# Performance work log

Hardware: AMD Instinct MI355X
Metric: run time of the kernel (lower is better)

Reference implementation:

```python
import jax, jax.numpy as jnp
import numpy as np

N_NODES = 50000
N_EDGES = 800000
IN_DIM, HID, EMB = 128, 256, 128


def _gcn_conv(x, src, dst, W, b, n_nodes):
    # PyG GCNConv: add self-loops, symmetric norm D^-1/2 (A+I) D^-1/2, then linear.
    h = x @ W  # [N, out]
    deg = jnp.zeros((n_nodes,), x.dtype).at[dst].add(1.0) + 1.0  # +1 for self-loop
    dinv = jax.lax.rsqrt(deg)
    norm = dinv[src] * dinv[dst]  # [E]
    agg = jnp.zeros_like(h).at[dst].add(h[src] * norm[:, None])
    agg = agg + h * (dinv * dinv)[:, None]  # self-loop term
    return agg + b


def setup_inputs() -> dict:
    key = jax.random.key(0)
    ks = jax.random.split(key, 16)
    s = lambda *sh: None
    x = jax.random.normal(ks[0], (N_NODES, IN_DIM), jnp.float32)
    edge_index = jax.random.randint(ks[1], (2, N_EDGES), 0, N_NODES, jnp.int32)
    def lin(k, fan_in, fan_out):
        lim = 1.0 / np.sqrt(fan_in)
        kw, kb = jax.random.split(k)
        W = jax.random.uniform(kw, (fan_in, fan_out), jnp.float32, -lim, lim)
        b = jax.random.uniform(kb, (fan_out,), jnp.float32, -lim, lim)
        return W, b
    W1, b1 = lin(ks[2], IN_DIM, HID)
    W2, b2 = lin(ks[3], HID, EMB)
    fc1_W, fc1_b = lin(ks[4], EMB, HID)
    fc2_W, fc2_b = lin(ks[5], HID, 1)
    np_W, np_b = lin(ks[6], EMB, 3)
    ep_W, ep_b = lin(ks[7], 2 * EMB, 2)
    gp_W, gp_b = lin(ks[8], EMB, 1)
    return dict(x=x, edge_index=edge_index, W1=W1, b1=b1, W2=W2, b2=b2,
                fc1_W=fc1_W, fc1_b=fc1_b, fc2_W=fc2_W, fc2_b=fc2_b,
                np_W=np_W, np_b=np_b, ep_W=ep_W, ep_b=ep_b, gp_W=gp_W, gp_b=gp_b)


def reference(x, edge_index, W1, b1, W2, b2, fc1_W, fc1_b, fc2_W, fc2_b,
              np_W, np_b, ep_W, ep_b, gp_W, gp_b):
    src, dst = edge_index[0], edge_index[1]
    n = x.shape[0]
    h = jax.nn.relu(_gcn_conv(x, src, dst, W1, b1, n))
    h = jax.nn.relu(_gcn_conv(h, src, dst, W2, b2, n))  # [N, EMB]
    g = jnp.mean(h, axis=0, keepdims=True)  # [1, EMB]
    v = jax.nn.relu(g @ fc1_W + fc1_b)
    value = v @ fc2_W + fc2_b  # [1,1]
    node_logits = h @ np_W + np_b  # [N,3]
    edge_features = jnp.concatenate([h[src], h[dst]], axis=1)  # [E, 2*EMB]
    edge_logits = edge_features @ ep_W + ep_b  # [E,2]
    global_logits = g @ gp_W + gp_b  # [1,1]
    return (node_logits, edge_logits, global_logits, value)
```

## Files before the change

### kernel.cpp

```cpp
#include <hip/hip_runtime.h>
#include <hip/hip_bf16.h>

typedef __attribute__((ext_vector_type(8))) short bf16x8;
typedef __attribute__((ext_vector_type(4))) float f32x4;

__device__ inline unsigned short f2bf(float f) {
    union { float f; unsigned u; } v; v.f = f;
    unsigned r = v.u + 0x7fff + ((v.u >> 16) & 1);
    return (unsigned short)(r >> 16);
}
__device__ inline float bf2f(unsigned short b) {
    union { unsigned u; float f; } v; v.u = ((unsigned)b) << 16;
    return v.f;
}
__device__ inline float bfu_lo(unsigned r) {
    union { unsigned u; float f; } v; v.u = r << 16;
    return v.f;
}
__device__ inline float bfu_hi(unsigned r) {
    union { unsigned u; float f; } v; v.u = r & 0xffff0000u;
    return v.f;
}

__global__ __launch_bounds__(256) void prep_kernel(
    const float* __restrict__ x, unsigned short* __restrict__ xb,
    const float* __restrict__ W1, unsigned short* __restrict__ W1t_hi, unsigned short* __restrict__ W1t_lo,
    const float* __restrict__ W2, unsigned short* __restrict__ W2t_hi, unsigned short* __restrict__ W2t_lo,
    int* __restrict__ zero_ints, float* __restrict__ gsum, int n) {
    int tid = blockIdx.x * blockDim.x + threadIdx.x;
    int C = n * 32;
    if (tid < C) {
        int base = tid * 4;
        float4 v = *(const float4*)&x[base];
        unsigned lo = (unsigned)f2bf(v.x) | ((unsigned)f2bf(v.y) << 16);
        unsigned hi = (unsigned)f2bf(v.z) | ((unsigned)f2bf(v.w) << 16);
        uint2 p; p.x = lo; p.y = hi;
        *(uint2*)&xb[base] = p;
        return;
    }
    tid -= C;
    if (tid < 65536) {
        if (tid < 32768) {
            int k = tid >> 8, j = tid & 255;
            float v = W1[tid];
            unsigned short h = f2bf(v);
            W1t_hi[(size_t)j * 128 + k] = h;
            W1t_lo[(size_t)j * 128 + k] = f2bf(v - bf2f(h));
        } else {
            int i2 = tid - 32768;
            int k = i2 >> 7, j = i2 & 127;
            float v = W2[i2];
            unsigned short h = f2bf(v);
            W2t_hi[(size_t)j * 256 + k] = h;
            W2t_lo[(size_t)j * 256 + k] = f2bf(v - bf2f(h));
        }
        return;
    }
    tid -= 65536;
    if (tid < 2 * n) { zero_ints[tid] = 0; return; }
    tid -= 2 * n;
    if (tid < 128) gsum[tid] = 0.f;
}

__global__ void hist_kernel(const int* __restrict__ dst, int* __restrict__ deg, int nE) {
    int e = blockIdx.x * blockDim.x + threadIdx.x;
    if (e < nE) atomicAdd(&deg[dst[e]], 1);
}

__global__ __launch_bounds__(1024) void scanA_kernel(const int* __restrict__ deg,
                                                     int* __restrict__ local,
                                                     float* __restrict__ dinv,
                                                     int* __restrict__ bsum, int n) {
    __shared__ int wsum[16];
    __shared__ int woff[16];
    int t = threadIdx.x, lane = t & 63, wid = t >> 6;
    int i = blockIdx.x * 1024 + t;
    int val = (i < n) ? deg[i] : 0;
    if (i < n) dinv[i] = rsqrtf((float)(val + 1));
    int inc = val;
    for (int s = 1; s < 64; s <<= 1) {
        int tmp = __shfl_up(inc, s);
        if (lane >= s) inc += tmp;
    }
    if (lane == 63) wsum[wid] = inc;
    __syncthreads();
    if (wid == 0) {
        int w = (lane < 16) ? wsum[lane] : 0;
        for (int s = 1; s < 16; s <<= 1) {
            int tmp = __shfl_up(w, s);
            if (lane >= s) w += tmp;
        }
        if (lane < 16) woff[lane] = w - wsum[lane];
        if (lane == 15) bsum[blockIdx.x] = w;
    }
    __syncthreads();
    if (i < n) local[i] = woff[wid] + (inc - val);
}

__global__ void scanB_kernel(const int* __restrict__ bsum, int* __restrict__ boff, int nb) {
    int lane = threadIdx.x & 63;
    int v = (lane < nb) ? bsum[lane] : 0;
    int inc = v;
    for (int s = 1; s < 64; s <<= 1) {
        int tmp = __shfl_up(inc, s);
        if (lane >= s) inc += tmp;
    }
    if (lane < nb) boff[lane] = inc - v;
}

__global__ void fill_kernel(const int* __restrict__ src, const int* __restrict__ dst,
                            const int* __restrict__ local, const int* __restrict__ boff,
                            int* __restrict__ cnt, const float* __restrict__ dinv,
                            int2* __restrict__ csr, int nE) {
    int e = blockIdx.x * blockDim.x + threadIdx.x;
    if (e >= nE) return;
    int s = src[e], d = dst[e];
    int pos = local[d] + boff[d >> 10] + atomicAdd(&cnt[d], 1);
    float w = dinv[s] * dinv[d];
    csr[pos] = make_int2(s, __float_as_int(w));
}

__global__ __launch_bounds__(256) void gather1_kernel(const unsigned int* __restrict__ xb,
                                                      const int2* __restrict__ csr,
                                                      const int* __restrict__ local,
                                                      const int* __restrict__ boff,
                                                      const int* __restrict__ deg,
                                                      const float* __restrict__ dinv,
                                                      unsigned int* __restrict__ xin_hi,
                                                      unsigned int* __restrict__ xin_lo, int n) {
    int node = blockIdx.x * 4 + (threadIdx.x >> 6);
    int lane = threadIdx.x & 63;
    if (node >= n) return;
    int p = local[node] + boff[node >> 10];
    int e0 = p + deg[node];
    unsigned rs = xb[(size_t)node * 64 + lane];
    float a0 = 0.f, a1 = 0.f, b0 = 0.f, b1 = 0.f;
    float c0 = 0.f, c1 = 0.f, d0v = 0.f, d1v = 0.f;
    for (; p + 7 < e0; p += 8) {
        int2 q0 = csr[p], q1 = csr[p + 1], q2 = csr[p + 2], q3 = csr[p + 3];
        int2 q4 = csr[p + 4], q5 = csr[p + 5], q6 = csr[p + 6], q7 = csr[p + 7];
        unsigned r0 = xb[(size_t)q0.x * 64 + lane];
        unsigned r1 = xb[(size_t)q1.x * 64 + lane];
        unsigned r2 = xb[(size_t)q2.x * 64 + lane];
        unsigned r3 = xb[(size_t)q3.x * 64 + lane];
        unsigned r4 = xb[(size_t)q4.x * 64 + lane];
        unsigned r5 = xb[(size_t)q5.x * 64 + lane];
        unsigned r6 = xb[(size_t)q6.x * 64 + lane];
        unsigned r7 = xb[(size_t)q7.x * 64 + lane];
        float w0 = __int_as_float(q0.y), w1 = __int_as_float(q1.y);
        float w2 = __int_as_float(q2.y), w3 = __int_as_float(q3.y);
        float w4 = __int_as_float(q4.y), w5 = __int_as_float(q5.y);
        float w6 = __int_as_float(q6.y), w7 = __int_as_float(q7.y);
        a0 += w0 * bfu_lo(r0); a1 += w0 * bfu_hi(r0);
        b0 += w1 * bfu_lo(r1); b1 += w1 * bfu_hi(r1);
        c0 += w2 * bfu_lo(r2); c1 += w2 * bfu_hi(r2);
        d0v += w3 * bfu_lo(r3); d1v += w3 * bfu_hi(r3);
        a0 += w4 * bfu_lo(r4); a1 += w4 * bfu_hi(r4);
        b0 += w5 * bfu_lo(r5); b1 += w5 * bfu_hi(r5);
        c0 += w6 * bfu_lo(r6); c1 += w6 * bfu_hi(r6);
        d0v += w7 * bfu_lo(r7); d1v += w7 * bfu_hi(r7);
    }
    for (; p + 3 < e0; p += 4) {
        int2 q0 = csr[p], q1 = csr[p + 1], q2 = csr[p + 2], q3 = csr[p + 3];
        unsigned r0 = xb[(size_t)q0.x * 64 + lane];
        unsigned r1 = xb[(size_t)q1.x * 64 + lane];
        unsigned r2 = xb[(size_t)q2.x * 64 + lane];
        unsigned r3 = xb[(size_t)q3.x * 64 + lane];
        float w0 = __int_as_float(q0.y), w1 = __int_as_float(q1.y);
        float w2 = __int_as_float(q2.y), w3 = __int_as_float(q3.y);
        a0 += w0 * bfu_lo(r0); a1 += w0 * bfu_hi(r0);
        b0 += w1 * bfu_lo(r1); b1 += w1 * bfu_hi(r1);
        c0 += w2 * bfu_lo(r2); c1 += w2 * bfu_hi(r2);
        d0v += w3 * bfu_lo(r3); d1v += w3 * bfu_hi(r3);
    }
    for (; p < e0; ++p) {
        int2 q = csr[p];
        float w = __int_as_float(q.y);
        unsigned r = xb[(size_t)q.x * 64 + lane];
        a0 += w * bfu_lo(r); a1 += w * bfu_hi(r);
    }
    a0 = (a0 + b0) + (c0 + d0v);
    a1 = (a1 + b1) + (c1 + d1v);
    float di = dinv[node];
    float d2 = di * di;
    a0 += d2 * bfu_lo(rs);
    a1 += d2 * bfu_hi(rs);
    unsigned short h0 = f2bf(a0), h1 = f2bf(a1);
    xin_hi[(size_t)node * 64 + lane] = (unsigned)h0 | ((unsigned)h1 << 16);
    unsigned short l0 = f2bf(a0 - bf2f(h0)), l1 = f2bf(a1 - bf2f(h1));
    xin_lo[(size_t)node * 64 + lane] = (unsigned)l0 | ((unsigned)l1 << 16);
}

template <int K, int NOUT, bool BIAS_RELU, bool A_SPLIT>
__global__ __launch_bounds__(256) void mfma_gemm_kernel(
    const unsigned short* __restrict__ Ahi, const unsigned short* __restrict__ Alo,
    const unsigned short* __restrict__ Wthi, const unsigned short* __restrict__ Wtlo,
    const float* __restrict__ bias,
    unsigned short* __restrict__ O, int n) {
    int w = threadIdx.x >> 6, l = threadIdx.x & 63;
    int m0 = blockIdx.x * 128 + w * 32;
    int j0 = blockIdx.y * 64;
    int col16 = l & 15;
    int koff = (l >> 4) * 8;
    int rowA0 = m0 + col16;       if (rowA0 >= n) rowA0 = n - 1;
    int rowA1 = m0 + 16 + col16;  if (rowA1 >= n) rowA1 = n - 1;
    f32x4 acc[2][4];
#pragma unroll
    for (int g = 0; g < 2; ++g)
#pragma unroll
        for (int c = 0; c < 4; ++c) acc[g][c] = (f32x4){0.f, 0.f, 0.f, 0.f};
    for (int k0 = 0; k0 < K; k0 += 32) {
        bf16x8 ah0 = *(const bf16x8*)&Ahi[(size_t)rowA0 * K + k0 + koff];
        bf16x8 ah1 = *(const bf16x8*)&Ahi[(size_t)rowA1 * K + k0 + koff];
        bf16x8 al0, al1;
        if (A_SPLIT) {
            al0 = *(const bf16x8*)&Alo[(size_t)rowA0 * K + k0 + koff];
            al1 = *(const bf16x8*)&Alo[(size_t)rowA1 * K + k0 + koff];
        }
#pragma unroll
        for (int c = 0; c < 4; ++c) {
            size_t wb = (size_t)(j0 + c * 16 + col16) * K + k0 + koff;
            bf16x8 wh = *(const bf16x8*)&Wthi[wb];
            bf16x8 wl = *(const bf16x8*)&Wtlo[wb];
            acc[0][c] = __builtin_amdgcn_mfma_f32_16x16x32_bf16(ah0, wh, acc[0][c], 0, 0, 0);
            if (A_SPLIT) acc[0][c] = __builtin_amdgcn_mfma_f32_16x16x32_bf16(al0, wh, acc[0][c], 0, 0, 0);
            acc[0][c] = __builtin_amdgcn_mfma_f32_16x16x32_bf16(ah0, wl, acc[0][c], 0, 0, 0);
            acc[1][c] = __builtin_amdgcn_mfma_f32_16x16x32_bf16(ah1, wh, acc[1][c], 0, 0, 0);
            if (A_SPLIT) acc[1][c] = __builtin_amdgcn_mfma_f32_16x16x32_bf16(al1, wh, acc[1][c], 0, 0, 0);
            acc[1][c] = __builtin_amdgcn_mfma_f32_16x16x32_bf16(ah1, wl, acc[1][c], 0, 0, 0);
        }
    }
#pragma unroll
    for (int g = 0; g < 2; ++g) {
#pragma unroll
        for (int c = 0; c < 4; ++c) {
            int col = j0 + c * 16 + col16;
#pragma unroll
            for (int r = 0; r < 4; ++r) {
                int orow = m0 + g * 16 + (l >> 4) * 4 + r;
                if (orow >= n) continue;
                float v = acc[g][c][r];
                if (BIAS_RELU) v = fmaxf(v + bias[col], 0.f);
                O[(size_t)orow * NOUT + col] = f2bf(v);
            }
        }
    }
}

__global__ __launch_bounds__(256) void conv2_fused_kernel(
    const unsigned int* __restrict__ h2b, const int2* __restrict__ csr,
    const int* __restrict__ local, const int* __restrict__ boff,
    const int* __restrict__ deg,
    const float* __restrict__ dinv, const float* __restrict__ b2,
    const float* __restrict__ npW, const float* __restrict__ npb,
    const float* __restrict__ epW, const float* __restrict__ epb,
    float* __restrict__ out_nl, float* __restrict__ uv,
    float* __restrict__ gsum, int n) {
    __shared__ float lgs[4][128];
    int lane = threadIdx.x & 63;
    int wid = threadIdx.x >> 6;
    int d0 = lane * 2, d1 = lane * 2 + 1;
    float wn00 = npW[d0 * 3 + 0], wn10 = npW[d0 * 3 + 1], wn20 = npW[d0 * 3 + 2];
    float wn01 = npW[d1 * 3 + 0], wn11 = npW[d1 * 3 + 1], wn21 = npW[d1 * 3 + 2];
    float wu00 = epW[d0 * 2 + 0], wu10 = epW[d0 * 2 + 1];
    float wu01 = epW[d1 * 2 + 0], wu11 = epW[d1 * 2 + 1];
    float wv00 = epW[(d0 + 128) * 2 + 0], wv10 = epW[(d0 + 128) * 2 + 1];
    float wv01 = epW[(d1 + 128) * 2 + 0], wv11 = epW[(d1 + 128) * 2 + 1];
    float b20 = b2[d0], b21 = b2[d1];
    float npb0 = npb[0], npb1 = npb[1], npb2 = npb[2];
    float epb0 = epb[0], epb1 = epb[1];
    float p0 = 0.f, p1 = 0.f;

    for (int node = blockIdx.x * 4 + wid; node < n; node += gridDim.x * 4) {
        int p = local[node] + boff[node >> 10];
        int e0 = p + deg[node];
        unsigned rs = h2b[(size_t)node * 64 + lane];
        float a0 = 0.f, a1 = 0.f, b0 = 0.f, b1 = 0.f;
        float c0 = 0.f, c1 = 0.f, e0v = 0.f, e1v = 0.f;
        for (; p + 7 < e0; p += 8) {
            int2 q0 = csr[p], q1 = csr[p + 1], q2 = csr[p + 2], q3 = csr[p + 3];
            int2 q4 = csr[p + 4], q5 = csr[p + 5], q6 = csr[p + 6], q7 = csr[p + 7];
            unsigned r0 = h2b[(size_t)q0.x * 64 + lane];
            unsigned r1 = h2b[(size_t)q1.x * 64 + lane];
            unsigned r2 = h2b[(size_t)q2.x * 64 + lane];
            unsigned r3 = h2b[(size_t)q3.x * 64 + lane];
            unsigned r4 = h2b[(size_t)q4.x * 64 + lane];
            unsigned r5 = h2b[(size_t)q5.x * 64 + lane];
            unsigned r6 = h2b[(size_t)q6.x * 64 + lane];
            unsigned r7 = h2b[(size_t)q7.x * 64 + lane];
            float w0 = __int_as_float(q0.y), w1 = __int_as_float(q1.y);
            float w2 = __int_as_float(q2.y), w3 = __int_as_float(q3.y);
            float w4 = __int_as_float(q4.y), w5 = __int_as_float(q5.y);
            float w6 = __int_as_float(q6.y), w7 = __int_as_float(q7.y);
            a0 += w0 * bfu_lo(r0); a1 += w0 * bfu_hi(r0);
            b0 += w1 * bfu_lo(r1); b1 += w1 * bfu_hi(r1);
            c0 += w2 * bfu_lo(r2); c1 += w2 * bfu_hi(r2);
            e0v += w3 * bfu_lo(r3); e1v += w3 * bfu_hi(r3);
            a0 += w4 * bfu_lo(r4); a1 += w4 * bfu_hi(r4);
            b0 += w5 * bfu_lo(r5); b1 += w5 * bfu_hi(r5);
            c0 += w6 * bfu_lo(r6); c1 += w6 * bfu_hi(r6);
            e0v += w7 * bfu_lo(r7); e1v += w7 * bfu_hi(r7);
        }
        for (; p + 3 < e0; p += 4) {
            int2 q0 = csr[p], q1 = csr[p + 1], q2 = csr[p + 2], q3 = csr[p + 3];
            unsigned r0 = h2b[(size_t)q0.x * 64 + lane];
            unsigned r1 = h2b[(size_t)q1.x * 64 + lane];
            unsigned r2 = h2b[(size_t)q2.x * 64 + lane];
            unsigned r3 = h2b[(size_t)q3.x * 64 + lane];
            float w0 = __int_as_float(q0.y), w1 = __int_as_float(q1.y);
            float w2 = __int_as_float(q2.y), w3 = __int_as_float(q3.y);
            a0 += w0 * bfu_lo(r0); a1 += w0 * bfu_hi(r0);
            b0 += w1 * bfu_lo(r1); b1 += w1 * bfu_hi(r1);
            c0 += w2 * bfu_lo(r2); c1 += w2 * bfu_hi(r2);
            e0v += w3 * bfu_lo(r3); e1v += w3 * bfu_hi(r3);
        }
        for (; p < e0; ++p) {
            int2 q = csr[p];
            float w = __int_as_float(q.y);
            unsigned r = h2b[(size_t)q.x * 64 + lane];
            a0 += w * bfu_lo(r); a1 += w * bfu_hi(r);
        }
        a0 = (a0 + b0) + (c0 + e0v);
        a1 = (a1 + b1) + (c1 + e1v);
        float di = dinv[node];
        float d2 = di * di;
        a0 = fmaxf(a0 + d2 * bfu_lo(rs) + b20, 0.f);
        a1 = fmaxf(a1 + d2 * bfu_hi(rs) + b21, 0.f);
        p0 += a0;
        p1 += a1;
        float n0 = a0 * wn00 + a1 * wn01;
        float n1 = a0 * wn10 + a1 * wn11;
        float n2 = a0 * wn20 + a1 * wn21;
        float u0 = a0 * wu00 + a1 * wu01;
        float u1 = a0 * wu10 + a1 * wu11;
        float v0 = a0 * wv00 + a1 * wv01;
        float v1 = a0 * wv10 + a1 * wv11;
        for (int off = 32; off; off >>= 1) {
            n0 += __shfl_xor(n0, off);
            n1 += __shfl_xor(n1, off);
            n2 += __shfl_xor(n2, off);
            u0 += __shfl_xor(u0, off);
            u1 += __shfl_xor(u1, off);
            v0 += __shfl_xor(v0, off);
            v1 += __shfl_xor(v1, off);
        }
        if (lane == 0) {
            out_nl[(size_t)node * 3 + 0] = n0 + npb0;
            out_nl[(size_t)node * 3 + 1] = n1 + npb1;
            out_nl[(size_t)node * 3 + 2] = n2 + npb2;
            float4 o;
            o.x = u0 + epb0; o.y = u1 + epb1; o.z = v0; o.w = v1;
            *(float4*)&uv[(size_t)node * 4] = o;
        }
    }
    lgs[wid][d0] = p0;
    lgs[wid][d1] = p1;
    __syncthreads();
    int t = threadIdx.x;
    if (t < 128) {
        float tot = lgs[0][t] + lgs[1][t] + lgs[2][t] + lgs[3][t];
        atomicAdd(&gsum[t], tot);
    }
}

__global__ __launch_bounds__(256) void edge_head_kernel(
    const float* __restrict__ uv, const int* __restrict__ src, const int* __restrict__ dst,
    float* __restrict__ out_el, int nE,
    const float* __restrict__ gsum,
    const float* __restrict__ fc1W, const float* __restrict__ fc1b,
    const float* __restrict__ fc2W, const float* __restrict__ fc2b,
    const float* __restrict__ gpW, const float* __restrict__ gpb,
    float* __restrict__ out_gl, float* __restrict__ out_val, int n) {
    if (blockIdx.x == 0) {
        __shared__ float g[128];
        __shared__ float red[256];
        int t = threadIdx.x;
        if (t < 128) g[t] = gsum[t] * (1.0f / (float)n);
        __syncthreads();
        float v = fc1b[t];
#pragma unroll
        for (int k = 0; k < 128; ++k) v += g[k] * fc1W[k * 256 + t];
        v = fmaxf(v, 0.0f);
        red[t] = v * fc2W[t];
        __syncthreads();
        for (int s = 128; s > 0; s >>= 1) { if (t < s) red[t] += red[t + s]; __syncthreads(); }
        if (t == 0) out_val[0] = red[0] + fc2b[0];
        __syncthreads();
        red[t] = (t < 128) ? g[t] * gpW[t] : 0.0f;
        __syncthreads();
        for (int s = 128; s > 0; s >>= 1) { if (t < s) red[t] += red[t + s]; __syncthreads(); }
        if (t == 0) out_gl[0] = red[0] + gpb[0];
        return;
    }
    int e = (blockIdx.x - 1) * blockDim.x + threadIdx.x;
    if (e >= nE) return;
    int s = src[e], d = dst[e];
    float2 u = *(const float2*)&uv[(size_t)s * 4];
    float2 v = *(const float2*)&uv[(size_t)d * 4 + 2];
    float2 o; o.x = u.x + v.x; o.y = u.y + v.y;
    *(float2*)&out_el[(size_t)e * 2] = o;
}

extern "C" void kernel_launch(void* const* d_in, const int* in_sizes, int n_in,
                              void* d_out, int out_size, void* d_ws, size_t ws_size,
                              hipStream_t stream) {
    const float* x    = (const float*)d_in[0];
    const int*   ei   = (const int*)d_in[1];
    const float* W1   = (const float*)d_in[2];
    const float* b1   = (const float*)d_in[3];
    const float* W2   = (const float*)d_in[4];
    const float* b2   = (const float*)d_in[5];
    const float* fc1W = (const float*)d_in[6];
    const float* fc1b = (const float*)d_in[7];
    const float* fc2W = (const float*)d_in[8];
    const float* fc2b = (const float*)d_in[9];
    const float* npW  = (const float*)d_in[10];
    const float* npb  = (const float*)d_in[11];
    const float* epW  = (const float*)d_in[12];
    const float* epb  = (const float*)d_in[13];
    const float* gpW  = (const float*)d_in[14];
    const float* gpb  = (const float*)d_in[15];
    float* out = (float*)d_out;

    const int n = in_sizes[0] / 128;
    const int E = in_sizes[1] / 2;
    const int* src = ei;
    const int* dst = ei + E;
    const int nb = (n + 1023) / 1024;

    char* p = (char*)d_ws;
    auto alloc = [&](size_t bytes) { char* r = p; p += (bytes + 255) & ~(size_t)255; return r; };
    unsigned short* xb     = (unsigned short*)alloc((size_t)n * 128 * 2);
    unsigned short* xin_hi = (unsigned short*)alloc((size_t)n * 128 * 2);
    unsigned short* xin_lo = (unsigned short*)alloc((size_t)n * 128 * 2);
    unsigned short* h      = (unsigned short*)alloc((size_t)n * 256 * 2);
    unsigned short* W1t_hi = (unsigned short*)alloc(128 * 256 * 2);
    unsigned short* W1t_lo = (unsigned short*)alloc(128 * 256 * 2);
    unsigned short* W2t_hi = (unsigned short*)alloc(256 * 128 * 2);
    unsigned short* W2t_lo = (unsigned short*)alloc(256 * 128 * 2);
    int2*  csr    = (int2*)alloc((size_t)E * 8);
    int*   deg    = (int*)alloc((size_t)n * 4 * 2);
    int*   cnt    = deg + n;
    int*   local  = (int*)alloc((size_t)n * 4);
    int*   bsum   = (int*)alloc(64 * 4);
    int*   boff   = (int*)alloc(64 * 4);
    float* dinv   = (float*)alloc((size_t)n * 4);
    float* uv     = (float*)alloc((size_t)n * 16);
    float* gsum   = (float*)alloc(512);
    unsigned short* h2b = xb;

    float* out_nl  = out;
    float* out_el  = out + (size_t)n * 3;
    float* out_gl  = out + (size_t)n * 3 + (size_t)E * 2;
    float* out_val = out_gl + 1;

    {
        long total = (long)n * 32 + 65536 + 2L * n + 128;
        int blocks = (int)((total + 255) / 256);
        prep_kernel<<<blocks, 256, 0, stream>>>(x, xb, W1, W1t_hi, W1t_lo,
                                                W2, W2t_hi, W2t_lo, deg, gsum, n);
    }

    hist_kernel<<<(E + 255) / 256, 256, 0, stream>>>(dst, deg, E);
    scanA_kernel<<<nb, 1024, 0, stream>>>(deg, local, dinv, bsum, n);
    scanB_kernel<<<1, 64, 0, stream>>>(bsum, boff, nb);
    fill_kernel<<<(E + 255) / 256, 256, 0, stream>>>(src, dst, local, boff, cnt, dinv, csr, E);

    gather1_kernel<<<(n + 3) / 4, 256, 0, stream>>>((const unsigned int*)xb, csr, local, boff,
                                                    deg, dinv, (unsigned int*)xin_hi,
                                                    (unsigned int*)xin_lo, n);

    dim3 g1((n + 127) / 128, 256 / 64);
    mfma_gemm_kernel<128, 256, true, true><<<g1, 256, 0, stream>>>(xin_hi, xin_lo, W1t_hi, W1t_lo,
                                                                   b1, h, n);
    dim3 g2((n + 127) / 128, 128 / 64);
    mfma_gemm_kernel<256, 128, false, false><<<g2, 256, 0, stream>>>(h, nullptr, W2t_hi, W2t_lo,
                                                                     nullptr, h2b, n);

    conv2_fused_kernel<<<2048, 256, 0, stream>>>((const unsigned int*)h2b, csr, local, boff,
                                                 deg, dinv, b2, npW, npb, epW, epb,
                                                 out_nl, uv, gsum, n);

    edge_head_kernel<<<1 + (E + 255) / 256, 256, 0, stream>>>(uv, src, dst, out_el, E,
                                                              gsum, fc1W, fc1b, fc2W, fc2b,
                                                              gpW, gpb, out_gl, out_val, n);
}
```

Before: 407.1 us.

## Gather neighbor rows with 16-byte loads across four edges per wave

Both CSR aggregation kernels are restructured so each wave splits into four 16-lane groups. Each group handles one edge at a time and each lane loads a 16-byte slice of the neighbor row. CSR entries are fetched once per 16 edges and broadcast with shuffles; partial sums are combined with cross-group shuffle reductions. The aim is to cut per-edge load instructions and raise memory-level parallelism. In exchange it adds shuffle and reduction overhead, wastes lanes on low-degree tails, and routes the conv2 result through LDS to return to the two-features-per-lane layout. Launch bounds are also tightened to ask for higher occupancy.

```diff
diff --git a/kernel.cpp b/kernel.cpp
--- a/kernel.cpp
+++ b/kernel.cpp
@@ -120,75 +120,75 @@
     csr[pos] = make_int2(s, __float_as_int(w));
 }
 
-__global__ __launch_bounds__(256) void gather1_kernel(const unsigned int* __restrict__ xb,
-                                                      const int2* __restrict__ csr,
-                                                      const int* __restrict__ local,
-                                                      const int* __restrict__ boff,
-                                                      const int* __restrict__ deg,
-                                                      const float* __restrict__ dinv,
-                                                      unsigned int* __restrict__ xin_hi,
-                                                      unsigned int* __restrict__ xin_lo, int n) {
+__global__ __launch_bounds__(256, 4) void gather1_kernel(const unsigned int* __restrict__ xb,
+                                                         const int2* __restrict__ csr,
+                                                         const int* __restrict__ local,
+                                                         const int* __restrict__ boff,
+                                                         const int* __restrict__ deg,
+                                                         const float* __restrict__ dinv,
+                                                         unsigned int* __restrict__ xin_hi,
+                                                         unsigned int* __restrict__ xin_lo, int n) {
     int node = blockIdx.x * 4 + (threadIdx.x >> 6);
     int lane = threadIdx.x & 63;
     if (node >= n) return;
-    int p = local[node] + boff[node >> 10];
-    int e0 = p + deg[node];
-    unsigned rs = xb[(size_t)node * 64 + lane];
-    float a0 = 0.f, a1 = 0.f, b0 = 0.f, b1 = 0.f;
-    float c0 = 0.f, c1 = 0.f, d0v = 0.f, d1v = 0.f;
-    for (; p + 7 < e0; p += 8) {
-        int2 q0 = csr[p], q1 = csr[p + 1], q2 = csr[p + 2], q3 = csr[p + 3];
-        int2 q4 = csr[p + 4], q5 = csr[p + 5], q6 = csr[p + 6], q7 = csr[p + 7];
-        unsigned r0 = xb[(size_t)q0.x * 64 + lane];
-        unsigned r1 = xb[(size_t)q1.x * 64 + lane];
-        unsigned r2 = xb[(size_t)q2.x * 64 + lane];
-        unsigned r3 = xb[(size_t)q3.x * 64 + lane];
-        unsigned r4 = xb[(size_t)q4.x * 64 + lane];
-        unsigned r5 = xb[(size_t)q5.x * 64 + lane];
-        unsigned r6 = xb[(size_t)q6.x * 64 + lane];
-        unsigned r7 = xb[(size_t)q7.x * 64 + lane];
-        float w0 = __int_as_float(q0.y), w1 = __int_as_float(q1.y);
-        float w2 = __int_as_float(q2.y), w3 = __int_as_float(q3.y);
-        float w4 = __int_as_float(q4.y), w5 = __int_as_float(q5.y);
-        float w6 = __int_as_float(q6.y), w7 = __int_as_float(q7.y);
-        a0 += w0 * bfu_lo(r0); a1 += w0 * bfu_hi(r0);
-        b0 += w1 * bfu_lo(r1); b1 += w1 * bfu_hi(r1);
-        c0 += w2 * bfu_lo(r2); c1 += w2 * bfu_hi(r2);
-        d0v += w3 * bfu_lo(r3); d1v += w3 * bfu_hi(r3);
-        a0 += w4 * bfu_lo(r4); a1 += w4 * bfu_hi(r4);
-        b0 += w5 * bfu_lo(r5); b1 += w5 * bfu_hi(r5);
-        c0 += w6 * bfu_lo(r6); c1 += w6 * bfu_hi(r6);
-        d0v += w7 * bfu_lo(r7); d1v += w7 * bfu_hi(r7);
-    }
-    for (; p + 3 < e0; p += 4) {
-        int2 q0 = csr[p], q1 = csr[p + 1], q2 = csr[p + 2], q3 = csr[p + 3];
-        unsigned r0 = xb[(size_t)q0.x * 64 + lane];
-        unsigned r1 = xb[(size_t)q1.x * 64 + lane];
-        unsigned r2 = xb[(size_t)q2.x * 64 + lane];
-        unsigned r3 = xb[(size_t)q3.x * 64 + lane];
-        float w0 = __int_as_float(q0.y), w1 = __int_as_float(q1.y);
-        float w2 = __int_as_float(q2.y), w3 = __int_as_float(q3.y);
-        a0 += w0 * bfu_lo(r0); a1 += w0 * bfu_hi(r0);
-        b0 += w1 * bfu_lo(r1); b1 += w1 * bfu_hi(r1);
-        c0 += w2 * bfu_lo(r2); c1 += w2 * bfu_hi(r2);
-        d0v += w3 * bfu_lo(r3); d1v += w3 * bfu_hi(r3);
-    }
-    for (; p < e0; ++p) {
-        int2 q = csr[p];
-        float w = __int_as_float(q.y);
-        unsigned r = xb[(size_t)q.x * 64 + lane];
-        a0 += w * bfu_lo(r); a1 += w * bfu_hi(r);
-    }
-    a0 = (a0 + b0) + (c0 + d0v);
-    a1 = (a1 + b1) + (c1 + d1v);
+    int sub = lane >> 4;
+    int seg = lane & 15;
+    int pstart = local[node] + boff[node >> 10];
+    int dg = deg[node];
+    int e0 = pstart + dg;
+    float acc[8] = {0.f, 0.f, 0.f, 0.f, 0.f, 0.f, 0.f, 0.f};
+    if (dg > 0) {
+        for (int b = pstart; b < e0; b += 16) {
+            int ci = b + (lane >> 2);
+            int2 q = csr[ci < e0 ? ci : e0 - 1];
+            float qw = __int_as_float(q.y);
+#pragma unroll
+            for (int j = 0; j < 4; ++j) {
+                if (b + 4 * j < e0) {
+                    int sl = 16 * j + 4 * sub;
+                    int   sj = __shfl(q.x, sl);
+                    float wj = __shfl(qw, sl);
+                    if (b + 4 * j + sub >= e0) wj = 0.f;
+                    uint4 r = *(const uint4*)(xb + (size_t)sj * 64 + (seg << 2));
+                    acc[0] += wj * bfu_lo(r.x); acc[1] += wj * bfu_hi(r.x);
+                    acc[2] += wj * bfu_lo(r.y); acc[3] += wj * bfu_hi(r.y);
+                    acc[4] += wj * bfu_lo(r.z); acc[5] += wj * bfu_hi(r.z);
+                    acc[6] += wj * bfu_lo(r.w); acc[7] += wj * bfu_hi(r.w);
+                }
+            }
+        }
+#pragma unroll
+        for (int j = 0; j < 8; ++j) {
+            acc[j] += __shfl_xor(acc[j], 16);
+            acc[j] += __shfl_xor(acc[j], 32);
+        }
+    }
     float di = dinv[node];
     float d2 = di * di;
-    a0 += d2 * bfu_lo(rs);
-    a1 += d2 * bfu_hi(rs);
-    unsigned short h0 = f2bf(a0), h1 = f2bf(a1);
-    xin_hi[(size_t)node * 64 + lane] = (unsigned)h0 | ((unsigned)h1 << 16);
-    unsigned short l0 = f2bf(a0 - bf2f(h0)), l1 = f2bf(a1 - bf2f(h1));
-    xin_lo[(size_t)node * 64 + lane] = (unsigned)l0 | ((unsigned)l1 << 16);
+    uint4 rs = *(const uint4*)(xb + (size_t)node * 64 + (seg << 2));
+    acc[0] += d2 * bfu_lo(rs.x); acc[1] += d2 * bfu_hi(rs.x);
+    acc[2] += d2 * bfu_lo(rs.y); acc[3] += d2 * bfu_hi(rs.y);
+    acc[4] += d2 * bfu_lo(rs.z); acc[5] += d2 * bfu_hi(rs.z);
+    acc[6] += d2 * bfu_lo(rs.w); acc[7] += d2 * bfu_hi(rs.w);
+    if (lane < 16) {
+        unsigned short hb[8], lb[8];
+#pragma unroll
+        for (int j = 0; j < 8; ++j) {
+            hb[j] = f2bf(acc[j]);
+            lb[j] = f2bf(acc[j] - bf2f(hb[j]));
+        }
+        uint4 ho, lo;
+        ho.x = (unsigned)hb[0] | ((unsigned)hb[1] << 16);
+        ho.y = (unsigned)hb[2] | ((unsigned)hb[3] << 16);
+        ho.z = (unsigned)hb[4] | ((unsigned)hb[5] << 16);
+        ho.w = (unsigned)hb[6] | ((unsigned)hb[7] << 16);
+        lo.x = (unsigned)lb[0] | ((unsigned)lb[1] << 16);
+        lo.y = (unsigned)lb[2] | ((unsigned)lb[3] << 16);
+        lo.z = (unsigned)lb[4] | ((unsigned)lb[5] << 16);
+        lo.w = (unsigned)lb[6] | ((unsigned)lb[7] << 16);
+        *(uint4*)(xin_hi + (size_t)node * 64 + (seg << 2)) = ho;
+        *(uint4*)(xin_lo + (size_t)node * 64 + (seg << 2)) = lo;
+    }
 }
 
 template <int K, int NOUT, bool BIAS_RELU, bool A_SPLIT>
@@ -247,7 +247,7 @@
     }
 }
 
-__global__ __launch_bounds__(256) void conv2_fused_kernel(
+__global__ __launch_bounds__(256, 4) void conv2_fused_kernel(
     const unsigned int* __restrict__ h2b, const int2* __restrict__ csr,
     const int* __restrict__ local, const int* __restrict__ boff,
     const int* __restrict__ deg,
@@ -257,8 +257,11 @@
     float* __restrict__ out_nl, float* __restrict__ uv,
     float* __restrict__ gsum, int n) {
     __shared__ float lgs[4][128];
+    __shared__ float bounce[4][128];
     int lane = threadIdx.x & 63;
     int wid = threadIdx.x >> 6;
+    int sub = lane >> 4;
+    int seg = lane & 15;
     int d0 = lane * 2, d1 = lane * 2 + 1;
     float wn00 = npW[d0 * 3 + 0], wn10 = npW[d0 * 3 + 1], wn20 = npW[d0 * 3 + 2];
     float wn01 = npW[d1 * 3 + 0], wn11 = npW[d1 * 3 + 1], wn21 = npW[d1 * 3 + 2];
@@ -272,60 +275,47 @@
     float p0 = 0.f, p1 = 0.f;
 
     for (int node = blockIdx.x * 4 + wid; node < n; node += gridDim.x * 4) {
-        int p = local[node] + boff[node >> 10];
-        int e0 = p + deg[node];
-        unsigned rs = h2b[(size_t)node * 64 + lane];
-        float a0 = 0.f, a1 = 0.f, b0 = 0.f, b1 = 0.f;
-        float c0 = 0.f, c1 = 0.f, e0v = 0.f, e1v = 0.f;
-        for (; p + 7 < e0; p += 8) {
-            int2 q0 = csr[p], q1 = csr[p + 1], q2 = csr[p + 2], q3 = csr[p + 3];
-            int2 q4 = csr[p + 4], q5 = csr[p + 5], q6 = csr[p + 6], q7 = csr[p + 7];
-            unsigned r0 = h2b[(size_t)q0.x * 64 + lane];
-            unsigned r1 = h2b[(size_t)q1.x * 64 + lane];
-            unsigned r2 = h2b[(size_t)q2.x * 64 + lane];
-            unsigned r3 = h2b[(size_t)q3.x * 64 + lane];
-            unsigned r4 = h2b[(size_t)q4.x * 64 + lane];
-            unsigned r5 = h2b[(size_t)q5.x * 64 + lane];
-            unsigned r6 = h2b[(size_t)q6.x * 64 + lane];
-            unsigned r7 = h2b[(size_t)q7.x * 64 + lane];
-            float w0 = __int_as_float(q0.y), w1 = __int_as_float(q1.y);
-            float w2 = __int_as_float(q2.y), w3 = __int_as_float(q3.y);
-            float w4 = __int_as_float(q4.y), w5 = __int_as_float(q5.y);
-            float w6 = __int_as_float(q6.y), w7 = __int_as_float(q7.y);
-            a0 += w0 * bfu_lo(r0); a1 += w0 * bfu_hi(r0);
-            b0 += w1 * bfu_lo(r1); b1 += w1 * bfu_hi(r1);
-            c0 += w2 * bfu_lo(r2); c1 += w2 * bfu_hi(r2);
-            e0v += w3 * bfu_lo(r3); e1v += w3 * bfu_hi(r3);
-            a0 += w4 * bfu_lo(r4); a1 += w4 * bfu_hi(r4);
-            b0 += w5 * bfu_lo(r5); b1 += w5 * bfu_hi(r5);
-            c0 += w6 * bfu_lo(r6); c1 += w6 * bfu_hi(r6);
-            e0v += w7 * bfu_lo(r7); e1v += w7 * bfu_hi(r7);
-        }
-        for (; p + 3 < e0; p += 4) {
-            int2 q0 = csr[p], q1 = csr[p + 1], q2 = csr[p + 2], q3 = csr[p + 3];
-            unsigned r0 = h2b[(size_t)q0.x * 64 + lane];
-            unsigned r1 = h2b[(size_t)q1.x * 64 + lane];
-            unsigned r2 = h2b[(size_t)q2.x * 64 + lane];
-            unsigned r3 = h2b[(size_t)q3.x * 64 + lane];
-            float w0 = __int_as_float(q0.y), w1 = __int_as_float(q1.y);
-            float w2 = __int_as_float(q2.y), w3 = __int_as_float(q3.y);
-            a0 += w0 * bfu_lo(r0); a1 += w0 * bfu_hi(r0);
-            b0 += w1 * bfu_lo(r1); b1 += w1 * bfu_hi(r1);
-            c0 += w2 * bfu_lo(r2); c1 += w2 * bfu_hi(r2);
-            e0v += w3 * bfu_lo(r3); e1v += w3 * bfu_hi(r3);
-        }
-        for (; p < e0; ++p) {
-            int2 q = csr[p];
-            float w = __int_as_float(q.y);
-            unsigned r = h2b[(size_t)q.x * 64 + lane];
-            a0 += w * bfu_lo(r); a1 += w * bfu_hi(r);
-        }
-        a0 = (a0 + b0) + (c0 + e0v);
-        a1 = (a1 + b1) + (c1 + e1v);
+        int pstart = local[node] + boff[node >> 10];
+        int dg = deg[node];
+        int e0 = pstart + dg;
+        float acc[8] = {0.f, 0.f, 0.f, 0.f, 0.f, 0.f, 0.f, 0.f};
+        if (dg > 0) {
+            for (int b = pstart; b < e0; b += 16) {
+                int ci = b + (lane >> 2);
+                int2 q = csr[ci < e0 ? ci : e0 - 1];
+                float qw = __int_as_float(q.y);
+#pragma unroll
+                for (int j = 0; j < 4; ++j) {
+                    if (b + 4 * j < e0) {
+                        int sl = 16 * j + 4 * sub;
+                        int   sj = __shfl(q.x, sl);
+                        float wj = __shfl(qw, sl);
+                        if (b + 4 * j + sub >= e0) wj = 0.f;
+                        uint4 r = *(const uint4*)(h2b + (size_t)sj * 64 + (seg << 2));
+                        acc[0] += wj * bfu_lo(r.x); acc[1] += wj * bfu_hi(r.x);
+                        acc[2] += wj * bfu_lo(r.y); acc[3] += wj * bfu_hi(r.y);
+                        acc[4] += wj * bfu_lo(r.z); acc[5] += wj * bfu_hi(r.z);
+                        acc[6] += wj * bfu_lo(r.w); acc[7] += wj * bfu_hi(r.w);
+                    }
+                }
+            }
+#pragma unroll
+            for (int j = 0; j < 8; ++j) {
+                acc[j] += __shfl_xor(acc[j], 16);
+                acc[j] += __shfl_xor(acc[j], 32);
+            }
+        }
+        if (lane < 16) {
+            *(float4*)&bounce[wid][lane * 8]     = make_float4(acc[0], acc[1], acc[2], acc[3]);
+            *(float4*)&bounce[wid][lane * 8 + 4] = make_float4(acc[4], acc[5], acc[6], acc[7]);
+        }
+        float2 ag = *(float2*)&bounce[wid][d0];
+        float a0 = ag.x, a1 = ag.y;
         float di = dinv[node];
         float d2 = di * di;
-        a0 = fmaxf(a0 + d2 * bfu_lo(rs) + b20, 0.f);
-        a1 = fmaxf(a1 + d2 * bfu_hi(rs) + b21, 0.f);
+        unsigned rsu = h2b[(size_t)node * 64 + lane];
+        a0 = fmaxf(a0 + d2 * bfu_lo(rsu) + b20, 0.f);
+        a1 = fmaxf(a1 + d2 * bfu_hi(rsu) + b21, 0.f);
         p0 += a0;
         p1 += a1;
         float n0 = a0 * wn00 + a1 * wn01;
```

Result: slower. 415.3 us (+2.0%).

## Edge-balanced node partitioning for gathers and wider GEMM column tiles

Applied to the files above, without the earlier changes.

Both gather kernels now give each wavefront a contiguous node range holding about the same number of edges, found by binary search over CSR offsets, in place of one node per wave or a strided loop. The aim is to even out work across waves and cut wave launch overhead. Separately, the MFMA GEMM now computes 128 output columns per block instead of 64, so each A tile is loaded half as often, at the cost of more accumulator registers and fewer blocks. The binary search adds a startup cost to every wave, and the sequential per-wave node loop may lower memory-level parallelism.

```diff
diff --git a/kernel.cpp b/kernel.cpp
--- a/kernel.cpp
+++ b/kernel.cpp
@@ -20,6 +20,17 @@
 __device__ inline float bfu_hi(unsigned r) {
     union { unsigned u; float f; } v; v.u = r & 0xffff0000u;
     return v.f;
+}
+
+__device__ inline int lbound(const int* __restrict__ local, const int* __restrict__ boff,
+                             int n, int target) {
+    int lo = 0, hi = n;
+    while (lo < hi) {
+        int m = (lo + hi) >> 1;
+        int sv = local[m] + boff[m >> 10];
+        if (sv < target) lo = m + 1; else hi = m;
+    }
+    return lo;
 }
 
 __global__ __launch_bounds__(256) void prep_kernel(
@@ -127,68 +138,74 @@
                                                       const int* __restrict__ deg,
                                                       const float* __restrict__ dinv,
                                                       unsigned int* __restrict__ xin_hi,
-                                                      unsigned int* __restrict__ xin_lo, int n) {
-    int node = blockIdx.x * 4 + (threadIdx.x >> 6);
+                                                      unsigned int* __restrict__ xin_lo,
+                                                      int n, int E) {
+    int wid = threadIdx.x >> 6;
     int lane = threadIdx.x & 63;
-    if (node >= n) return;
-    int p = local[node] + boff[node >> 10];
-    int e0 = p + deg[node];
-    unsigned rs = xb[(size_t)node * 64 + lane];
-    float a0 = 0.f, a1 = 0.f, b0 = 0.f, b1 = 0.f;
-    float c0 = 0.f, c1 = 0.f, d0v = 0.f, d1v = 0.f;
-    for (; p + 7 < e0; p += 8) {
-        int2 q0 = csr[p], q1 = csr[p + 1], q2 = csr[p + 2], q3 = csr[p + 3];
-        int2 q4 = csr[p + 4], q5 = csr[p + 5], q6 = csr[p + 6], q7 = csr[p + 7];
-        unsigned r0 = xb[(size_t)q0.x * 64 + lane];
-        unsigned r1 = xb[(size_t)q1.x * 64 + lane];
-        unsigned r2 = xb[(size_t)q2.x * 64 + lane];
-        unsigned r3 = xb[(size_t)q3.x * 64 + lane];
-        unsigned r4 = xb[(size_t)q4.x * 64 + lane];
-        unsigned r5 = xb[(size_t)q5.x * 64 + lane];
-        unsigned r6 = xb[(size_t)q6.x * 64 + lane];
-        unsigned r7 = xb[(size_t)q7.x * 64 + lane];
-        float w0 = __int_as_float(q0.y), w1 = __int_as_float(q1.y);
-        float w2 = __int_as_float(q2.y), w3 = __int_as_float(q3.y);
-        float w4 = __int_as_float(q4.y), w5 = __int_as_float(q5.y);
-        float w6 = __int_as_float(q6.y), w7 = __int_as_float(q7.y);
-        a0 += w0 * bfu_lo(r0); a1 += w0 * bfu_hi(r0);
-        b0 += w1 * bfu_lo(r1); b1 += w1 * bfu_hi(r1);
-        c0 += w2 * bfu_lo(r2); c1 += w2 * bfu_hi(r2);
-        d0v += w3 * bfu_lo(r3); d1v += w3 * bfu_hi(r3);
-        a0 += w4 * bfu_lo(r4); a1 += w4 * bfu_hi(r4);
-        b0 += w5 * bfu_lo(r5); b1 += w5 * bfu_hi(r5);
-        c0 += w6 * bfu_lo(r6); c1 += w6 * bfu_hi(r6);
-        d0v += w7 * bfu_lo(r7); d1v += w7 * bfu_hi(r7);
-    }
-    for (; p + 3 < e0; p += 4) {
-        int2 q0 = csr[p], q1 = csr[p + 1], q2 = csr[p + 2], q3 = csr[p + 3];
-        unsigned r0 = xb[(size_t)q0.x * 64 + lane];
-        unsigned r1 = xb[(size_t)q1.x * 64 + lane];
-        unsigned r2 = xb[(size_t)q2.x * 64 + lane];
-        unsigned r3 = xb[(size_t)q3.x * 64 + lane];
-        float w0 = __int_as_float(q0.y), w1 = __int_as_float(q1.y);
-        float w2 = __int_as_float(q2.y), w3 = __int_as_float(q3.y);
-        a0 += w0 * bfu_lo(r0); a1 += w0 * bfu_hi(r0);
-        b0 += w1 * bfu_lo(r1); b1 += w1 * bfu_hi(r1);
-        c0 += w2 * bfu_lo(r2); c1 += w2 * bfu_hi(r2);
-        d0v += w3 * bfu_lo(r3); d1v += w3 * bfu_hi(r3);
-    }
-    for (; p < e0; ++p) {
-        int2 q = csr[p];
-        float w = __int_as_float(q.y);
-        unsigned r = xb[(size_t)q.x * 64 + lane];
-        a0 += w * bfu_lo(r); a1 += w * bfu_hi(r);
-    }
-    a0 = (a0 + b0) + (c0 + d0v);
-    a1 = (a1 + b1) + (c1 + d1v);
-    float di = dinv[node];
-    float d2 = di * di;
-    a0 += d2 * bfu_lo(rs);
-    a1 += d2 * bfu_hi(rs);
-    unsigned short h0 = f2bf(a0), h1 = f2bf(a1);
-    xin_hi[(size_t)node * 64 + lane] = (unsigned)h0 | ((unsigned)h1 << 16);
-    unsigned short l0 = f2bf(a0 - bf2f(h0)), l1 = f2bf(a1 - bf2f(h1));
-    xin_lo[(size_t)node * 64 + lane] = (unsigned)l0 | ((unsigned)l1 << 16);
+    int W = gridDim.x * 4;
+    int w = blockIdx.x * 4 + wid;
+    int ns = lbound(local, boff, n, (int)((long)w * E / W));
+    int ne = (w == W - 1) ? n : lbound(local, boff, n, (int)((long)(w + 1) * E / W));
+    for (int node = ns; node < ne; ++node) {
+        int p = local[node] + boff[node >> 10];
+        int e0 = p + deg[node];
+        unsigned rs = xb[(size_t)node * 64 + lane];
+        float a0 = 0.f, a1 = 0.f, b0 = 0.f, b1 = 0.f;
+        float c0 = 0.f, c1 = 0.f, d0v = 0.f, d1v = 0.f;
+        for (; p + 7 < e0; p += 8) {
+            int2 q0 = csr[p], q1 = csr[p + 1], q2 = csr[p + 2], q3 = csr[p + 3];
+            int2 q4 = csr[p + 4], q5 = csr[p + 5], q6 = csr[p + 6], q7 = csr[p + 7];
+            unsigned r0 = xb[(size_t)q0.x * 64 + lane];
+            unsigned r1 = xb[(size_t)q1.x * 64 + lane];
+            unsigned r2 = xb[(size_t)q2.x * 64 + lane];
+            unsigned r3 = xb[(size_t)q3.x * 64 + lane];
+            unsigned r4 = xb[(size_t)q4.x * 64 + lane];
+            unsigned r5 = xb[(size_t)q5.x * 64 + lane];
+            unsigned r6 = xb[(size_t)q6.x * 64 + lane];
+            unsigned r7 = xb[(size_t)q7.x * 64 + lane];
+            float w0 = __int_as_float(q0.y), w1 = __int_as_float(q1.y);
+            float w2 = __int_as_float(q2.y), w3 = __int_as_float(q3.y);
+            float w4 = __int_as_float(q4.y), w5 = __int_as_float(q5.y);
+            float w6 = __int_as_float(q6.y), w7 = __int_as_float(q7.y);
+            a0 += w0 * bfu_lo(r0); a1 += w0 * bfu_hi(r0);
+            b0 += w1 * bfu_lo(r1); b1 += w1 * bfu_hi(r1);
+            c0 += w2 * bfu_lo(r2); c1 += w2 * bfu_hi(r2);
+            d0v += w3 * bfu_lo(r3); d1v += w3 * bfu_hi(r3);
+            a0 += w4 * bfu_lo(r4); a1 += w4 * bfu_hi(r4);
+            b0 += w5 * bfu_lo(r5); b1 += w5 * bfu_hi(r5);
+            c0 += w6 * bfu_lo(r6); c1 += w6 * bfu_hi(r6);
+            d0v += w7 * bfu_lo(r7); d1v += w7 * bfu_hi(r7);
+        }
+        for (; p + 3 < e0; p += 4) {
+            int2 q0 = csr[p], q1 = csr[p + 1], q2 = csr[p + 2], q3 = csr[p + 3];
+            unsigned r0 = xb[(size_t)q0.x * 64 + lane];
+            unsigned r1 = xb[(size_t)q1.x * 64 + lane];
+            unsigned r2 = xb[(size_t)q2.x * 64 + lane];
+            unsigned r3 = xb[(size_t)q3.x * 64 + lane];
+            float w0 = __int_as_float(q0.y), w1 = __int_as_float(q1.y);
+            float w2 = __int_as_float(q2.y), w3 = __int_as_float(q3.y);
+            a0 += w0 * bfu_lo(r0); a1 += w0 * bfu_hi(r0);
+            b0 += w1 * bfu_lo(r1); b1 += w1 * bfu_hi(r1);
+            c0 += w2 * bfu_lo(r2); c1 += w2 * bfu_hi(r2);
+            d0v += w3 * bfu_lo(r3); d1v += w3 * bfu_hi(r3);
+        }
+        for (; p < e0; ++p) {
+            int2 q = csr[p];
+            float ww = __int_as_float(q.y);
+            unsigned r = xb[(size_t)q.x * 64 + lane];
+            a0 += ww * bfu_lo(r); a1 += ww * bfu_hi(r);
+        }
+        a0 = (a0 + b0) + (c0 + d0v);
+        a1 = (a1 + b1) + (c1 + d1v);
+        float di = dinv[node];
+        float d2 = di * di;
+        a0 += d2 * bfu_lo(rs);
+        a1 += d2 * bfu_hi(rs);
+        unsigned short h0 = f2bf(a0), h1 = f2bf(a1);
+        xin_hi[(size_t)node * 64 + lane] = (unsigned)h0 | ((unsigned)h1 << 16);
+        unsigned short l0 = f2bf(a0 - bf2f(h0)), l1 = f2bf(a1 - bf2f(h1));
+        xin_lo[(size_t)node * 64 + lane] = (unsigned)l0 | ((unsigned)l1 << 16);
+    }
 }
 
 template <int K, int NOUT, bool BIAS_RELU, bool A_SPLIT>
@@ -199,16 +216,18 @@
     unsigned short* __restrict__ O, int n) {
     int w = threadIdx.x >> 6, l = threadIdx.x & 63;
     int m0 = blockIdx.x * 128 + w * 32;
-    int j0 = blockIdx.y * 64;
+    int j0 = blockIdx.y * 128;
     int col16 = l & 15;
     int koff = (l >> 4) * 8;
     int rowA0 = m0 + col16;       if (rowA0 >= n) rowA0 = n - 1;
     int rowA1 = m0 + 16 + col16;  if (rowA1 >= n) rowA1 = n - 1;
-    f32x4 acc[2][4];
+    f32x4 acc[2][2][4];
 #pragma unroll
     for (int g = 0; g < 2; ++g)
 #pragma unroll
-        for (int c = 0; c < 4; ++c) acc[g][c] = (f32x4){0.f, 0.f, 0.f, 0.f};
+        for (int jt = 0; jt < 2; ++jt)
+#pragma unroll
+            for (int c = 0; c < 4; ++c) acc[g][jt][c] = (f32x4){0.f, 0.f, 0.f, 0.f};
     for (int k0 = 0; k0 < K; k0 += 32) {
         bf16x8 ah0 = *(const bf16x8*)&Ahi[(size_t)rowA0 * K + k0 + koff];
         bf16x8 ah1 = *(const bf16x8*)&Ahi[(size_t)rowA1 * K + k0 + koff];
@@ -218,30 +237,36 @@
             al1 = *(const bf16x8*)&Alo[(size_t)rowA1 * K + k0 + koff];
         }
 #pragma unroll
-        for (int c = 0; c < 4; ++c) {
-            size_t wb = (size_t)(j0 + c * 16 + col16) * K + k0 + koff;
-            bf16x8 wh = *(const bf16x8*)&Wthi[wb];
-            bf16x8 wl = *(const bf16x8*)&Wtlo[wb];
-            acc[0][c] = __builtin_amdgcn_mfma_f32_16x16x32_bf16(ah0, wh, acc[0][c], 0, 0, 0);
-            if (A_SPLIT) acc[0][c] = __builtin_amdgcn_mfma_f32_16x16x32_bf16(al0, wh, acc[0][c], 0, 0, 0);
-            acc[0][c] = __builtin_amdgcn_mfma_f32_16x16x32_bf16(ah0, wl, acc[0][c], 0, 0, 0);
-            acc[1][c] = __builtin_amdgcn_mfma_f32_16x16x32_bf16(ah1, wh, acc[1][c], 0, 0, 0);
-            if (A_SPLIT) acc[1][c] = __builtin_amdgcn_mfma_f32_16x16x32_bf16(al1, wh, acc[1][c], 0, 0, 0);
-            acc[1][c] = __builtin_amdgcn_mfma_f32_16x16x32_bf16(ah1, wl, acc[1][c], 0, 0, 0);
+        for (int jt = 0; jt < 2; ++jt) {
+#pragma unroll
+            for (int c = 0; c < 4; ++c) {
+                size_t wb = (size_t)(j0 + jt * 64 + c * 16 + col16) * K + k0 + koff;
+                bf16x8 wh = *(const bf16x8*)&Wthi[wb];
+                bf16x8 wl = *(const bf16x8*)&Wtlo[wb];
+                acc[0][jt][c] = __builtin_amdgcn_mfma_f32_16x16x32_bf16(ah0, wh, acc[0][jt][c], 0, 0, 0);
+                if (A_SPLIT) acc[0][jt][c] = __builtin_amdgcn_mfma_f32_16x16x32_bf16(al0, wh, acc[0][jt][c], 0, 0, 0);
+                acc[0][jt][c] = __builtin_amdgcn_mfma_f32_16x16x32_bf16(ah0, wl, acc[0][jt][c], 0, 0, 0);
+                acc[1][jt][c] = __builtin_amdgcn_mfma_f32_16x16x32_bf16(ah1, wh, acc[1][jt][c], 0, 0, 0);
+                if (A_SPLIT) acc[1][jt][c] = __builtin_amdgcn_mfma_f32_16x16x32_bf16(al1, wh, acc[1][jt][c], 0, 0, 0);
+                acc[1][jt][c] = __builtin_amdgcn_mfma_f32_16x16x32_bf16(ah1, wl, acc[1][jt][c], 0, 0, 0);
+            }
         }
     }
 #pragma unroll
     for (int g = 0; g < 2; ++g) {
 #pragma unroll
-        for (int c = 0; c < 4; ++c) {
-            int col = j0 + c * 16 + col16;
-#pragma unroll
-            for (int r = 0; r < 4; ++r) {
-                int orow = m0 + g * 16 + (l >> 4) * 4 + r;
-                if (orow >= n) continue;
-                float v = acc[g][c][r];
-                if (BIAS_RELU) v = fmaxf(v + bias[col], 0.f);
-                O[(size_t)orow * NOUT + col] = f2bf(v);
+        for (int jt = 0; jt < 2; ++jt) {
+#pragma unroll
+            for (int c = 0; c < 4; ++c) {
+                int col = j0 + jt * 64 + c * 16 + col16;
+#pragma unroll
+                for (int r = 0; r < 4; ++r) {
+                    int orow = m0 + g * 16 + (l >> 4) * 4 + r;
+                    if (orow >= n) continue;
+                    float v = acc[g][jt][c][r];
+                    if (BIAS_RELU) v = fmaxf(v + bias[col], 0.f);
+                    O[(size_t)orow * NOUT + col] = f2bf(v);
+                }
             }
         }
     }
@@ -255,7 +280,7 @@
     const float* __restrict__ npW, const float* __restrict__ npb,
     const float* __restrict__ epW, const float* __restrict__ epb,
     float* __restrict__ out_nl, float* __restrict__ uv,
-    float* __restrict__ gsum, int n) {
+    float* __restrict__ gsum, int n, int E) {
     __shared__ float lgs[4][128];
     int lane = threadIdx.x & 63;
     int wid = threadIdx.x >> 6;
@@ -271,7 +296,11 @@
     float epb0 = epb[0], epb1 = epb[1];
     float p0 = 0.f, p1 = 0.f;
 
-    for (int node = blockIdx.x * 4 + wid; node < n; node += gridDim.x * 4) {
+    int W = gridDim.x * 4;
+    int w = blockIdx.x * 4 + wid;
+    int ns = lbound(local, boff, n, (int)((long)w * E / W));
+    int ne = (w == W - 1) ? n : lbound(local, boff, n, (int)((long)(w + 1) * E / W));
+    for (int node = ns; node < ne; ++node) {
         int p = local[node] + boff[node >> 10];
         int e0 = p + deg[node];
         unsigned rs = h2b[(size_t)node * 64 + lane];
@@ -316,9 +345,9 @@
         }
         for (; p < e0; ++p) {
             int2 q = csr[p];
-            float w = __int_as_float(q.y);
+            float ww = __int_as_float(q.y);
             unsigned r = h2b[(size_t)q.x * 64 + lane];
-            a0 += w * bfu_lo(r); a1 += w * bfu_hi(r);
+            a0 += ww * bfu_lo(r); a1 += ww * bfu_hi(r);
         }
         a0 = (a0 + b0) + (c0 + e0v);
         a1 = (a1 + b1) + (c1 + e1v);
@@ -466,20 +495,20 @@
     scanB_kernel<<<1, 64, 0, stream>>>(bsum, boff, nb);
     fill_kernel<<<(E + 255) / 256, 256, 0, stream>>>(src, dst, local, boff, cnt, dinv, csr, E);
 
-    gather1_kernel<<<(n + 3) / 4, 256, 0, stream>>>((const unsigned int*)xb, csr, local, boff,
-                                                    deg, dinv, (unsigned int*)xin_hi,
-                                                    (unsigned int*)xin_lo, n);
-
-    dim3 g1((n + 127) / 128, 256 / 64);
+    gather1_kernel<<<2048, 256, 0, stream>>>((const unsigned int*)xb, csr, local, boff,
+                                             deg, dinv, (unsigned int*)xin_hi,
+                                             (unsigned int*)xin_lo, n, E);
+
+    dim3 g1((n + 127) / 128, 2);
     mfma_gemm_kernel<128, 256, true, true><<<g1, 256, 0, stream>>>(xin_hi, xin_lo, W1t_hi, W1t_lo,
                                                                    b1, h, n);
-    dim3 g2((n + 127) / 128, 128 / 64);
+    dim3 g2((n + 127) / 128, 1);
     mfma_gemm_kernel<256, 128, false, false><<<g2, 256, 0, stream>>>(h, nullptr, W2t_hi, W2t_lo,
                                                                      nullptr, h2b, n);
 
     conv2_fused_kernel<<<2048, 256, 0, stream>>>((const unsigned int*)h2b, csr, local, boff,
                                                  deg, dinv, b2, npW, npb, epW, epb,
-                                                 out_nl, uv, gsum, n);
+                                                 out_nl, uv, gsum, n, E);
 
     edge_head_kernel<<<1 + (E + 255) / 256, 256, 0, stream>>>(uv, src, dst, out_el, E,
                                                               gsum, fc1W, fc1b, fc2W, fc2b,
```

New measurement: 426.9 us. +4.9%, slower.
